# Performance work log

Hardware: AMD Instinct MI355X
Metric: run time of the kernel (lower is better)

## Reference

```python
import jax, jax.numpy as jnp
import numpy as np

PI_2 = 3.14159 / 2  # matches the torch module's pi_2 constant
EPS = 1e-8          # F.cosine_similarity default eps


def setup_inputs() -> dict:
    key = jax.random.key(0)
    k1, k2 = jax.random.split(key)
    B, N, C, H, W = 32, 2000, 512, 7, 7
    key_t = jax.random.normal(k1, (B, C, H, W), dtype=jnp.float32)
    memory = jax.random.normal(k2, (N, C, H, W), dtype=jnp.float32)
    return {"key": key_t, "memory": memory}


def reference(key, memory):
    # Memory.read(key): cosine-similarity addressing + tan warp + softmax, then weighted read.
    B = key.shape[0]
    N = memory.shape[0]
    k = key.reshape(B, -1)        # [B, D], D = C*H*W
    m = memory.reshape(N, -1)     # [N, D]
    # cosine similarity with torch's eps clamping on norms
    dots = jnp.einsum('bd,nd->bn', k, m)                                   # [B, N]
    k_norm = jnp.maximum(jnp.sqrt(jnp.sum(k * k, axis=-1, keepdims=True)), EPS)  # [B, 1]
    m_norm = jnp.maximum(jnp.sqrt(jnp.sum(m * m, axis=-1)), EPS)                 # [N]
    cos = dots / (k_norm * m_norm[None, :])                                 # [B, N]
    w = jax.nn.softmax(jnp.tan(cos * PI_2), axis=1)                         # [B, N]
    # weighted read: sum_n w[b,n] * memory[n,c,h,w] -> [B, C, H, W]
    out = jnp.einsum('bn,nchw->bchw', w, memory)
    return out
```

## Files before the change

### kernel.cpp

```cpp
#include <hip/hip_runtime.h>
#include <math.h>

#define D_ELEMS 25088
#define D4      6272
#define N_MEM   2000
#define B_KEYS  32
#define PI_2F   1.570795f
#define EPSF    1e-8f
#define NSLICE  49
#define KSLICE  512
#define KSTEPS  16
#define NWAVES  (125 * NSLICE)
#define RTILE   100

using short8 = __attribute__((ext_vector_type(8))) short;
using short4v = __attribute__((ext_vector_type(4))) short;
using f32x4  = __attribute__((ext_vector_type(4))) float;


__device__ inline short f2bf(float x) {
    union { float f; unsigned u; } v; v.f = x;
    unsigned r = v.u + 0x7fffu + ((v.u >> 16) & 1u);
    return (short)(r >> 16);
}

__global__ __launch_bounds__(256) void k_prep(const float* __restrict__ key,
                                              short* __restrict__ keyb) {
    const int i = blockIdx.x * 256 + threadIdx.x;
    const float4 f = ((const float4*)key)[i];
    short4v s; s[0] = f2bf(f.x); s[1] = f2bf(f.y); s[2] = f2bf(f.z); s[3] = f2bf(f.w);
    ((short4v*)keyb)[i] = s;
}

__global__ __launch_bounds__(256) void k_knorm(const float* __restrict__ key,
                                               float* __restrict__ knorm) {
    const int b   = blockIdx.x;
    const int tid = threadIdx.x;
    const float4* K4 = (const float4*)(key + (size_t)b * D_ELEMS);
    float ks = 0.f;
    for (int i = tid; i < D4; i += 256) {
        const float4 f = K4[i];
        ks += f.x * f.x + f.y * f.y + f.z * f.z + f.w * f.w;
    }
#pragma unroll
    for (int o = 1; o < 64; o <<= 1) ks += __shfl_xor(ks, o, 64);
    __shared__ float sred[4];
    if ((tid & 63) == 0) sred[tid >> 6] = ks;
    __syncthreads();
    if (tid == 0)
        knorm[b] = fmaxf(sqrtf(sred[0] + sred[1] + sred[2] + sred[3]), EPSF);
}

__global__ __launch_bounds__(256) void k_dots_mfma(const short* __restrict__ keyb,
                                                  const float* __restrict__ mem,
                                                  float* __restrict__ dots_part,
                                                  float* __restrict__ mn2_part) {
    const int wid = blockIdx.x * 4 + (threadIdx.x >> 6);
    if (wid >= NWAVES) return;
    const int nt   = wid / NSLICE;
    const int s    = wid % NSLICE;
    const int n0   = nt * 16;
    const int lane = threadIdx.x & 63;
    const int quad = lane >> 4;
    const int l16  = lane & 15;
    const int k0   = s * KSLICE + quad * 8;

    const short* a0p = keyb + (size_t)l16 * D_ELEMS + k0;
    const short* a1p = keyb + (size_t)(16 + l16) * D_ELEMS + k0;
    const float4* bp = (const float4*)(mem + (size_t)(n0 + l16) * D_ELEMS + k0);

    f32x4 acc0 = {0.f, 0.f, 0.f, 0.f};
    f32x4 acc1 = {0.f, 0.f, 0.f, 0.f};
    float msq = 0.f;

    short8 a0 = *(const short8*)a0p;
    short8 a1 = *(const short8*)a1p;
    float4 f0 = bp[0], f1 = bp[1];

    for (int t = 0; t < KSTEPS; ++t) {
        const short8 a0c = a0, a1c = a1;
        const float4 f0c = f0, f1c = f1;
        if (t + 1 < KSTEPS) {
            a0 = *(const short8*)(a0p + (t + 1) * 32);
            a1 = *(const short8*)(a1p + (t + 1) * 32);
            f0 = bp[(t + 1) * 8];
            f1 = bp[(t + 1) * 8 + 1];
        }
        msq += f0c.x * f0c.x + f0c.y * f0c.y + f0c.z * f0c.z + f0c.w * f0c.w
             + f1c.x * f1c.x + f1c.y * f1c.y + f1c.z * f1c.z + f1c.w * f1c.w;
        short8 b;
        b[0] = f2bf(f0c.x); b[1] = f2bf(f0c.y); b[2] = f2bf(f0c.z); b[3] = f2bf(f0c.w);
        b[4] = f2bf(f1c.x); b[5] = f2bf(f1c.y); b[6] = f2bf(f1c.z); b[7] = f2bf(f1c.w);
        acc0 = __builtin_amdgcn_mfma_f32_16x16x32_bf16(a0c, b, acc0, 0, 0, 0);
        acc1 = __builtin_amdgcn_mfma_f32_16x16x32_bf16(a1c, b, acc1, 0, 0, 0);
    }

    float* dp = dots_part + (size_t)(s * N_MEM + n0 + l16) * B_KEYS;
#pragma unroll
    for (int r = 0; r < 4; ++r) {
        dp[quad * 4 + r]      = acc0[r];
        dp[16 + quad * 4 + r] = acc1[r];
    }

    msq += __shfl_xor(msq, 16, 64);
    msq += __shfl_xor(msq, 32, 64);
    if (lane < 16) mn2_part[s * N_MEM + n0 + lane] = msq;
}

__global__ __launch_bounds__(256) void k_reduce(const float* __restrict__ dots_part,
                                                const float* __restrict__ mn2_part,
                                                float* __restrict__ dots,
                                                float* __restrict__ mn2) {
    const int gid = blockIdx.x * 256 + threadIdx.x;
    float ds = 0.f;
#pragma unroll
    for (int s = 0; s < NSLICE; ++s) ds += dots_part[s * (N_MEM * B_KEYS) + gid];
    dots[gid] = ds;
    if (gid < N_MEM) {
        float ms = 0.f;
#pragma unroll
        for (int s = 0; s < NSLICE; ++s) ms += mn2_part[s * N_MEM + gid];
        mn2[gid] = ms;
    }
}

__global__ __launch_bounds__(512) void k_softmax(const float* __restrict__ knormArr,
                                                 const float* __restrict__ dots,
                                                 const float* __restrict__ mn2,
                                                 float* __restrict__ w) {
    const int b   = blockIdx.x;
    const int tid = threadIdx.x;
    __shared__ float sred[512];
    __shared__ float xbuf[N_MEM];
    const float knorm = knormArr[b];

    float mx = -1e30f;
    for (int n = tid; n < N_MEM; n += 512) {
        const float mn = fmaxf(sqrtf(mn2[n]), EPSF);
        const float x  = __tanf((dots[n * B_KEYS + b] / (knorm * mn)) * PI_2F);
        xbuf[n] = x;
        mx = fmaxf(mx, x);
    }
    sred[tid] = mx;
    __syncthreads();
    for (int o = 256; o; o >>= 1) {
        if (tid < o) sred[tid] = fmaxf(sred[tid], sred[tid + o]);
        __syncthreads();
    }
    mx = sred[0];
    __syncthreads();

    float sm = 0.f;
    for (int n = tid; n < N_MEM; n += 512) {
        const float e = __expf(xbuf[n] - mx);
        xbuf[n] = e;
        sm += e;
    }
    sred[tid] = sm;
    __syncthreads();
    for (int o = 256; o; o >>= 1) {
        if (tid < o) sred[tid] += sred[tid + o];
        __syncthreads();
    }
    const float inv = 1.f / sred[0];

    for (int n = tid; n < N_MEM; n += 512)
        w[n * B_KEYS + b] = xbuf[n] * inv;
}

__global__ __launch_bounds__(256, 2) void k_read(const float* __restrict__ mem,
                                                 const float* __restrict__ w,
                                                 float* __restrict__ partial,
                                                 int nPerS) {
    const int db   = blockIdx.x % 49;
    const int s    = blockIdx.x / 49;
    const int n0   = s * nPerS;
    const int lane = threadIdx.x & 63;
    const int wv   = threadIdx.x >> 6;
    const int bh   = wv & 1;
    const int dh   = wv >> 1;
    const int d4   = db * 128 + dh * 64 + lane;

    const float4* M4 = (const float4*)mem;
    const float4* W4 = (const float4*)w;
    __shared__ float4 wls[RTILE * 8];

    float acc[16][4];
#pragma unroll
    for (int i = 0; i < 16; ++i) {
        acc[i][0] = 0.f; acc[i][1] = 0.f; acc[i][2] = 0.f; acc[i][3] = 0.f;
    }

    for (int c0 = 0; c0 < nPerS; c0 += RTILE) {
        __syncthreads();
        for (int i = threadIdx.x; i < RTILE * 8; i += 256)
            wls[i] = W4[(size_t)(n0 + c0) * 8 + i];
        __syncthreads();

        const float4* mp = M4 + (size_t)(n0 + c0) * D4 + d4;
#pragma unroll 4
        for (int nn = 0; nn < RTILE; ++nn) {
            const float4 mc = mp[(size_t)nn * D4];
#pragma unroll
            for (int q = 0; q < 4; ++q) {
                const float4 wq = wls[nn * 8 + bh * 4 + q];
                const int b0 = q * 4;
                acc[b0+0][0] += wq.x * mc.x; acc[b0+0][1] += wq.x * mc.y;
                acc[b0+0][2] += wq.x * mc.z; acc[b0+0][3] += wq.x * mc.w;
                acc[b0+1][0] += wq.y * mc.x; acc[b0+1][1] += wq.y * mc.y;
                acc[b0+1][2] += wq.y * mc.z; acc[b0+1][3] += wq.y * mc.w;
                acc[b0+2][0] += wq.z * mc.x; acc[b0+2][1] += wq.z * mc.y;
                acc[b0+2][2] += wq.z * mc.z; acc[b0+2][3] += wq.z * mc.w;
                acc[b0+3][0] += wq.w * mc.x; acc[b0+3][1] += wq.w * mc.y;
                acc[b0+3][2] += wq.w * mc.z; acc[b0+3][3] += wq.w * mc.w;
            }
        }
    }

    float4* P4 = (float4*)partial;
#pragma unroll
    for (int b = 0; b < 16; ++b)
        P4[(size_t)(s * B_KEYS + bh * 16 + b) * D4 + d4] =
            make_float4(acc[b][0], acc[b][1], acc[b][2], acc[b][3]);
}

__global__ __launch_bounds__(256) void k_finish(const float* __restrict__ partial,
                                                float* __restrict__ out, int ns) {
    const int i = blockIdx.x * 256 + threadIdx.x;
    const float4* P4 = (const float4*)partial;
    float4 sum = P4[i];
    for (int s = 1; s < ns; ++s) {
        const float4 p = P4[(size_t)s * (B_KEYS * D4) + i];
        sum.x += p.x; sum.y += p.y; sum.z += p.z; sum.w += p.w;
    }
    ((float4*)out)[i] = sum;
}

extern "C" void kernel_launch(void* const* d_in, const int* in_sizes, int n_in,
                              void* d_out, int out_size, void* d_ws, size_t ws_size,
                              hipStream_t stream) {
    (void)in_sizes; (void)n_in; (void)out_size;
    const float* key = (const float*)d_in[0];
    const float* mem = (const float*)d_in[1];
    float* out = (float*)d_out;
    float* ws  = (float*)d_ws;

    short* keyb      = (short*)ws;
    float* dots_part = ws + 401408;
    float* mn2_part  = ws + 3537408;
    float* dots      = ws + 3635408;
    float* mn2       = ws + 3699408;
    float* knorm     = ws + 3701408;
    float* w         = ws + 3701440;
    float* part      = ws + 3765440;

    int ns = 20;
    while (ns > 1 && (size_t)(3765440 + (size_t)ns * 802816) * 4 > ws_size)
        ns = (ns == 20) ? 10 : (ns == 10) ? 5 : (ns == 5) ? 2 : 1;
    const int nPerS = N_MEM / ns;

    k_prep     <<<784, 256, 0, stream>>>(key, keyb);
    k_knorm    <<<B_KEYS, 256, 0, stream>>>(key, knorm);
    k_dots_mfma<<<(NWAVES + 3) / 4, 256, 0, stream>>>(keyb, mem, dots_part, mn2_part);
    k_reduce   <<<250, 256, 0, stream>>>(dots_part, mn2_part, dots, mn2);
    k_softmax  <<<B_KEYS, 512, 0, stream>>>(knorm, dots, mn2, w);
    k_read     <<<49 * ns, 256, 0, stream>>>(mem, w, part, nPerS);
    k_finish   <<<784, 256, 0, stream>>>(part, out, ns);
}
```

Before: 377.3 us.

## Restructure weighted read to split memory rows across waves with LDS reduction

The weighted-read kernel now has each wave hold all 32 keys for a 64-float4 column slice, with the four waves taking interleaved memory rows and combining their partials through an LDS reduction. A four-deep register prefetch of memory rows replaces the unrolled loop, the tile grows to 200 rows, and the N-split drops from 20 to 10, which halves partial traffic for the finish kernel. The dots kernel is relaunched with one wave per block. The goals are fewer partial writes and better latency hiding, at the cost of 128 accumulator registers per thread (spill/occupancy risk) and extra barriers.

```diff
diff --git a/kernel.cpp b/kernel.cpp
--- a/kernel.cpp
+++ b/kernel.cpp
@@ -10,8 +10,7 @@
 #define NSLICE  49
 #define KSLICE  512
 #define KSTEPS  16
-#define NWAVES  (125 * NSLICE)
-#define RTILE   100
+#define RTILE   200
 
 using short8 = __attribute__((ext_vector_type(8))) short;
 using short4v = __attribute__((ext_vector_type(4))) short;
@@ -51,16 +50,14 @@
         knorm[b] = fmaxf(sqrtf(sred[0] + sred[1] + sred[2] + sred[3]), EPSF);
 }
 
-__global__ __launch_bounds__(256) void k_dots_mfma(const short* __restrict__ keyb,
+__global__ __launch_bounds__(64) void k_dots_mfma(const short* __restrict__ keyb,
                                                   const float* __restrict__ mem,
                                                   float* __restrict__ dots_part,
                                                   float* __restrict__ mn2_part) {
-    const int wid = blockIdx.x * 4 + (threadIdx.x >> 6);
-    if (wid >= NWAVES) return;
-    const int nt   = wid / NSLICE;
-    const int s    = wid % NSLICE;
+    const int nt   = blockIdx.x / NSLICE;
+    const int s    = blockIdx.x % NSLICE;
     const int n0   = nt * 16;
-    const int lane = threadIdx.x & 63;
+    const int lane = threadIdx.x;
     const int quad = lane >> 4;
     const int l16  = lane & 15;
     const int k0   = s * KSLICE + quad * 8;
@@ -172,22 +169,23 @@
                                                  const float* __restrict__ w,
                                                  float* __restrict__ partial,
                                                  int nPerS) {
-    const int db   = blockIdx.x % 49;
-    const int s    = blockIdx.x / 49;
+    const int db   = blockIdx.x % 98;
+    const int s    = blockIdx.x / 98;
     const int n0   = s * nPerS;
     const int lane = threadIdx.x & 63;
     const int wv   = threadIdx.x >> 6;
-    const int bh   = wv & 1;
-    const int dh   = wv >> 1;
-    const int d4   = db * 128 + dh * 64 + lane;
+    const int d4   = db * 64 + lane;
 
     const float4* M4 = (const float4*)mem;
     const float4* W4 = (const float4*)w;
-    __shared__ float4 wls[RTILE * 8];
-
-    float acc[16][4];
-#pragma unroll
-    for (int i = 0; i < 16; ++i) {
+
+    __shared__ __align__(16) char smem[32768];
+    float4* wls = (float4*)smem;
+    float4 (*red)[8][64] = (float4 (*)[8][64])smem;
+
+    float acc[32][4];
+#pragma unroll
+    for (int i = 0; i < 32; ++i) {
         acc[i][0] = 0.f; acc[i][1] = 0.f; acc[i][2] = 0.f; acc[i][3] = 0.f;
     }
 
@@ -198,12 +196,18 @@
         __syncthreads();
 
         const float4* mp = M4 + (size_t)(n0 + c0) * D4 + d4;
-#pragma unroll 4
-        for (int nn = 0; nn < RTILE; ++nn) {
-            const float4 mc = mp[(size_t)nn * D4];
-#pragma unroll
-            for (int q = 0; q < 4; ++q) {
-                const float4 wq = wls[nn * 8 + bh * 4 + q];
+        float4 mv0 = mp[(size_t)(wv)      * D4];
+        float4 mv1 = mp[(size_t)(wv + 4)  * D4];
+        float4 mv2 = mp[(size_t)(wv + 8)  * D4];
+        float4 mv3 = mp[(size_t)(wv + 12) * D4];
+        for (int nn = wv; nn < RTILE; nn += 4) {
+            const float4 mc = mv0;
+            mv0 = mv1; mv1 = mv2; mv2 = mv3;
+            if (nn + 16 < RTILE)
+                mv3 = mp[(size_t)(nn + 16) * D4];
+#pragma unroll
+            for (int q = 0; q < 8; ++q) {
+                const float4 wq = wls[nn * 8 + q];
                 const int b0 = q * 4;
                 acc[b0+0][0] += wq.x * mc.x; acc[b0+0][1] += wq.x * mc.y;
                 acc[b0+0][2] += wq.x * mc.z; acc[b0+0][3] += wq.x * mc.w;
@@ -218,10 +222,26 @@
     }
 
     float4* P4 = (float4*)partial;
-#pragma unroll
-    for (int b = 0; b < 16; ++b)
-        P4[(size_t)(s * B_KEYS + bh * 16 + b) * D4 + d4] =
-            make_float4(acc[b][0], acc[b][1], acc[b][2], acc[b][3]);
+    const int col = threadIdx.x & 63;
+    const int jj  = threadIdx.x >> 6;
+#pragma unroll
+    for (int p = 0; p < 4; ++p) {
+        __syncthreads();
+#pragma unroll
+        for (int j = 0; j < 8; ++j)
+            red[wv][j][lane] = make_float4(acc[p*8+j][0], acc[p*8+j][1],
+                                           acc[p*8+j][2], acc[p*8+j][3]);
+        __syncthreads();
+#pragma unroll
+        for (int h = 0; h < 2; ++h) {
+            const int j = jj + h * 4;
+            const float4 a = red[0][j][col], b = red[1][j][col];
+            const float4 c = red[2][j][col], d = red[3][j][col];
+            P4[(size_t)(s * B_KEYS + p * 8 + j) * D4 + db * 64 + col] =
+                make_float4(a.x + b.x + c.x + d.x, a.y + b.y + c.y + d.y,
+                            a.z + b.z + c.z + d.z, a.w + b.w + c.w + d.w);
+        }
+    }
 }
 
 __global__ __launch_bounds__(256) void k_finish(const float* __restrict__ partial,
@@ -254,16 +274,16 @@
     float* w         = ws + 3701440;
     float* part      = ws + 3765440;
 
-    int ns = 20;
+    int ns = 10;
     while (ns > 1 && (size_t)(3765440 + (size_t)ns * 802816) * 4 > ws_size)
-        ns = (ns == 20) ? 10 : (ns == 10) ? 5 : (ns == 5) ? 2 : 1;
+        ns = (ns == 10) ? 5 : (ns == 5) ? 2 : 1;
     const int nPerS = N_MEM / ns;
 
     k_prep     <<<784, 256, 0, stream>>>(key, keyb);
     k_knorm    <<<B_KEYS, 256, 0, stream>>>(key, knorm);
-    k_dots_mfma<<<(NWAVES + 3) / 4, 256, 0, stream>>>(keyb, mem, dots_part, mn2_part);
+    k_dots_mfma<<<125 * NSLICE, 64, 0, stream>>>(keyb, mem, dots_part, mn2_part);
     k_reduce   <<<250, 256, 0, stream>>>(dots_part, mn2_part, dots, mn2);
     k_softmax  <<<B_KEYS, 512, 0, stream>>>(knorm, dots, mn2, w);
-    k_read     <<<49 * ns, 256, 0, stream>>>(mem, w, part, nPerS);
+    k_read     <<<98 * ns, 256, 0, stream>>>(mem, w, part, nPerS);
     k_finish   <<<784, 256, 0, stream>>>(part, out, ns);
 }
```

New measurement: 383.8 us. About the same (+1.7%).
